# Optimization experiments

Measured on AMD Instinct MI355X. Metric: run time of the kernel, lower is better.

Reference implementation:

```python
import jax, jax.numpy as jnp
import numpy as np

N_NODES = 200000  # graph size
D = 128           # feature dim == out_size
N1 = 81920        # layer-1 node set size
B = 8192          # batch size
K = 10            # num_sample neighbors


def setup_inputs() -> dict:
    key = jax.random.key(0)
    k = jax.random.split(key, 7)
    raw_features = jax.random.normal(k[0], (N_NODES, D), dtype=jnp.float32)
    # xavier-like scale for weights [out, 2*in]
    W1 = jax.random.normal(k[1], (D, 2 * D), dtype=jnp.float32) * (1.0 / np.sqrt(2 * D))
    W2 = jax.random.normal(k[2], (D, 2 * D), dtype=jnp.float32) * (1.0 / np.sqrt(2 * D))
    layer1_nodes = jax.random.randint(k[3], (N1,), 0, N_NODES)
    neigh0_idx = jax.random.randint(k[4], (N1, K), 0, N_NODES)
    map_batch = jax.random.randint(k[5], (B,), 0, N1)
    neigh1_idx = jax.random.randint(k[6], (B, K), 0, N1)
    return {
        "raw_features": raw_features,
        "W1": W1,
        "W2": W2,
        "layer1_nodes": layer1_nodes,
        "neigh0_idx": neigh0_idx,
        "map_batch": map_batch,
        "neigh1_idx": neigh1_idx,
    }


def _sage_layer(self_feats, agg_feats, W):
    # combined = cat([self, agg], dim=1); relu(W @ combined.T).T == relu(combined @ W.T)
    combined = jnp.concatenate([self_feats, agg_feats], axis=1)
    return jax.nn.relu(combined @ W.T)


def reference(raw_features, W1, W2, layer1_nodes, neigh0_idx, map_batch, neigh1_idx):
    # Layer 1: aggregate raw features over K sampled neighbors (MEAN), gcn=False
    agg0 = jnp.mean(raw_features[neigh0_idx], axis=1)        # [N1, D]
    self0 = raw_features[layer1_nodes]                        # [N1, D]
    h1 = _sage_layer(self0, agg0, W1)                         # [N1, D]
    # Layer 2: aggregate layer-1 embeddings for the batch nodes
    agg1 = jnp.mean(h1[neigh1_idx], axis=1)                   # [B, D]
    self1 = h1[map_batch]                                     # [B, D]
    h2 = _sage_layer(self1, agg1, W2)                         # [B, D]
    return h2
```

## Files before the change

### kernel.cpp

```cpp
#include <hip/hip_runtime.h>
#include <stdint.h>

#define D 128
#define K_NEI 10
#define TILE_M 64

typedef __bf16 bf16x8 __attribute__((ext_vector_type(8)));
typedef float f32x4 __attribute__((ext_vector_type(4)));

__device__ __forceinline__ uint32_t f2bf(float f) {
    union { float f; uint32_t u; } v; v.f = f;
    uint32_t u = v.u;
    return (u + 0x7FFFu + ((u >> 16) & 1u)) >> 16;
}
__device__ __forceinline__ float bf2f(uint32_t h) {
    union { uint32_t u; float f; } v; v.u = h << 16; return v.f;
}
__device__ __forceinline__ uint32_t pack2(float a, float b) {
    return f2bf(a) | (f2bf(b) << 16);
}

template <bool FEATS_F32>
__global__ void build_A(const void* __restrict__ feats_,
                        const int* __restrict__ self_idx,
                        const int* __restrict__ neigh_idx,
                        uint16_t* __restrict__ A, int M)
{
    const int t = blockIdx.x * 256 + threadIdx.x;
    const int i = t >> 4;
    const int j = t & 15;
    if (i >= M) return;

    const float*    ff = (const float*)feats_;
    const uint16_t* fb = (const uint16_t*)feats_;

    {
        int node = self_idx[i];
        uint4 o;
        if (FEATS_F32) {
            const float* src = ff + (size_t)node * D + j * 8;
            f32x4 a = *(const f32x4*)src;
            f32x4 b = *(const f32x4*)(src + 4);
            o.x = pack2(a[0], a[1]); o.y = pack2(a[2], a[3]);
            o.z = pack2(b[0], b[1]); o.w = pack2(b[2], b[3]);
        } else {
            o = *(const uint4*)(fb + (size_t)node * D + j * 8);
        }
        *(uint4*)(A + (size_t)i * 256 + j * 8) = o;
    }

    const int* nrow = neigh_idx + (size_t)i * K_NEI;
    int idx[K_NEI];
    #pragma unroll
    for (int k = 0; k < K_NEI; ++k) idx[k] = nrow[k];

    float s0=0,s1=0,s2=0,s3=0,s4=0,s5=0,s6=0,s7=0;
    #pragma unroll
    for (int k = 0; k < K_NEI; ++k) {
        if (FEATS_F32) {
            const float* src = ff + (size_t)idx[k] * D + j * 8;
            f32x4 a = *(const f32x4*)src;
            f32x4 b = *(const f32x4*)(src + 4);
            s0 += a[0]; s1 += a[1]; s2 += a[2]; s3 += a[3];
            s4 += b[0]; s5 += b[1]; s6 += b[2]; s7 += b[3];
        } else {
            uint4 v = *(const uint4*)(fb + (size_t)idx[k] * D + j * 8);
            s0 += bf2f(v.x & 0xFFFFu); s1 += bf2f(v.x >> 16);
            s2 += bf2f(v.y & 0xFFFFu); s3 += bf2f(v.y >> 16);
            s4 += bf2f(v.z & 0xFFFFu); s5 += bf2f(v.z >> 16);
            s6 += bf2f(v.w & 0xFFFFu); s7 += bf2f(v.w >> 16);
        }
    }
    const float inv = 0.1f;
    uint4 o;
    o.x = pack2(s0 * inv, s1 * inv);
    o.y = pack2(s2 * inv, s3 * inv);
    o.z = pack2(s4 * inv, s5 * inv);
    o.w = pack2(s6 * inv, s7 * inv);
    *(uint4*)(A + (size_t)i * 256 + 128 + j * 8) = o;
}

template <bool OUT_F32>
__global__ void gemm_relu(const uint16_t* __restrict__ A,
                          const float* __restrict__ W,
                          void* __restrict__ out_)
{
    __shared__ __align__(16) uint16_t Alds[TILE_M * 128];
    __shared__ __align__(16) uint16_t Wlds[128 * 128];

    const int tid  = threadIdx.x;
    const int wave = tid >> 6;
    const int lane = tid & 63;
    const int r16  = lane & 15;
    const int q    = lane >> 4;
    const int G    = blockIdx.x * TILE_M;

    f32x4 acc[8];
    #pragma unroll
    for (int nt = 0; nt < 8; ++nt) acc[nt] = (f32x4){0.f, 0.f, 0.f, 0.f};

    for (int half = 0; half < 2; ++half) {
        #pragma unroll
        for (int it = 0; it < 8; ++it) {
            int t = it * 256 + tid;
            int j = t >> 4, c = t & 15;
            const float* src = W + (size_t)j * 256 + half * 128 + c * 8;
            f32x4 w0 = *(const f32x4*)(src);
            f32x4 w1 = *(const f32x4*)(src + 4);
            uint4 o;
            o.x = pack2(w0[0], w0[1]); o.y = pack2(w0[2], w0[3]);
            o.z = pack2(w1[0], w1[1]); o.w = pack2(w1[2], w1[3]);
            int cs = c ^ (j & 15);
            *(uint4*)(Wlds + j * 128 + cs * 8) = o;
        }
        #pragma unroll
        for (int it = 0; it < 4; ++it) {
            int t = it * 256 + tid;
            int n = t >> 4, c = t & 15;
            uint4 v = *(const uint4*)(A + (size_t)(G + n) * 256 + half * 128 + c * 8);
            int cs = c ^ (n & 15);
            *(uint4*)(Alds + n * 128 + cs * 8) = v;
        }
        __syncthreads();

        #pragma unroll
        for (int ks = 0; ks < 4; ++ks) {
            int cidx = ks * 4 + q;
            bf16x8 a = *(const bf16x8*)(Alds + (wave * 16 + r16) * 128 + ((cidx ^ r16) * 8));
            bf16x8 b[8];
            #pragma unroll
            for (int nt = 0; nt < 8; ++nt) {
                int jj = nt * 16 + r16;
                b[nt] = *(const bf16x8*)(Wlds + jj * 128 + ((cidx ^ r16) * 8));
            }
            #pragma unroll
            for (int nt = 0; nt < 8; ++nt)
                acc[nt] = __builtin_amdgcn_mfma_f32_16x16x32_bf16(a, b[nt], acc[nt], 0, 0, 0);
        }
        __syncthreads();
    }

    const int row_base = G + wave * 16 + q * 4;
    #pragma unroll
    for (int nt = 0; nt < 8; ++nt) {
        int col = nt * 16 + r16;
        #pragma unroll
        for (int r = 0; r < 4; ++r) {
            float v = acc[nt][r];
            v = v > 0.f ? v : 0.f;
            if (OUT_F32) ((float*)out_)[(size_t)(row_base + r) * D + col] = v;
            else ((uint16_t*)out_)[(size_t)(row_base + r) * D + col] = (uint16_t)f2bf(v);
        }
    }
}

template <bool FEATS_F32, bool OUT_F32>
__global__ void sage_layer(const void* __restrict__ feats_,
                           const float* __restrict__ W,
                           const int* __restrict__ self_idx,
                           const int* __restrict__ neigh_idx,
                           void* __restrict__ out_)
{
    __shared__ __align__(16) uint16_t Alds[TILE_M * 128];
    __shared__ __align__(16) uint16_t Wlds[128 * 128];

    const int tid  = threadIdx.x;
    const int wave = tid >> 6;
    const int lane = tid & 63;
    const int r16  = lane & 15;
    const int q    = lane >> 4;
    const int G    = blockIdx.x * TILE_M;

    const float*    feats_f = (const float*)feats_;
    const uint16_t* feats_b = (const uint16_t*)feats_;

    f32x4 acc[8];
    #pragma unroll
    for (int nt = 0; nt < 8; ++nt) acc[nt] = (f32x4){0.f, 0.f, 0.f, 0.f};

    for (int half = 0; half < 2; ++half) {
        #pragma unroll
        for (int it = 0; it < 8; ++it) {
            int t = it * 256 + tid;
            int j = t >> 4, c = t & 15;
            const float* src = W + (size_t)j * 256 + half * 128 + c * 8;
            f32x4 w0 = *(const f32x4*)(src);
            f32x4 w1 = *(const f32x4*)(src + 4);
            uint4 o;
            o.x = pack2(w0[0], w0[1]); o.y = pack2(w0[2], w0[3]);
            o.z = pack2(w1[0], w1[1]); o.w = pack2(w1[2], w1[3]);
            int cs = c ^ (j & 15);
            *(uint4*)(Wlds + j * 128 + cs * 8) = o;
        }
        if (half == 0) {
            #pragma unroll
            for (int it = 0; it < 4; ++it) {
                int t = it * 256 + tid;
                int n = t >> 4, c = t & 15;
                int node = self_idx[G + n];
                uint4 o;
                if (FEATS_F32) {
                    const float* src = feats_f + (size_t)node * D + c * 8;
                    f32x4 f0 = *(const f32x4*)(src);
                    f32x4 f1 = *(const f32x4*)(src + 4);
                    o.x = pack2(f0[0], f0[1]); o.y = pack2(f0[2], f0[3]);
                    o.z = pack2(f1[0], f1[1]); o.w = pack2(f1[2], f1[3]);
                } else {
                    o = *(const uint4*)(feats_b + (size_t)node * D + c * 8);
                }
                int cs = c ^ (n & 15);
                *(uint4*)(Alds + n * 128 + cs * 8) = o;
            }
        } else {
            #pragma unroll
            for (int it = 0; it < 4; ++it) {
                int t = it * 256 + tid;
                int n = t >> 4, c = t & 15;
                const int* nrow = neigh_idx + (size_t)(G + n) * K_NEI;
                float s0=0,s1=0,s2=0,s3=0,s4=0,s5=0,s6=0,s7=0;
                #pragma unroll
                for (int k = 0; k < K_NEI; ++k) {
                    if (FEATS_F32) {
                        const float* src = feats_f + (size_t)nrow[k] * D + c * 8;
                        f32x4 f0 = *(const f32x4*)(src);
                        f32x4 f1 = *(const f32x4*)(src + 4);
                        s0 += f0[0]; s1 += f0[1]; s2 += f0[2]; s3 += f0[3];
                        s4 += f1[0]; s5 += f1[1]; s6 += f1[2]; s7 += f1[3];
                    } else {
                        uint4 v = *(const uint4*)(feats_b + (size_t)nrow[k] * D + c * 8);
                        s0 += bf2f(v.x & 0xFFFFu); s1 += bf2f(v.x >> 16);
                        s2 += bf2f(v.y & 0xFFFFu); s3 += bf2f(v.y >> 16);
                        s4 += bf2f(v.z & 0xFFFFu); s5 += bf2f(v.z >> 16);
                        s6 += bf2f(v.w & 0xFFFFu); s7 += bf2f(v.w >> 16);
                    }
                }
                const float inv = 0.1f;
                uint4 o;
                o.x = pack2(s0 * inv, s1 * inv);
                o.y = pack2(s2 * inv, s3 * inv);
                o.z = pack2(s4 * inv, s5 * inv);
                o.w = pack2(s6 * inv, s7 * inv);
                int cs = c ^ (n & 15);
                *(uint4*)(Alds + n * 128 + cs * 8) = o;
            }
        }
        __syncthreads();

        #pragma unroll
        for (int ks = 0; ks < 4; ++ks) {
            int cidx = ks * 4 + q;
            bf16x8 a = *(const bf16x8*)(Alds + (wave * 16 + r16) * 128 + ((cidx ^ r16) * 8));
            bf16x8 b[8];
            #pragma unroll
            for (int nt = 0; nt < 8; ++nt) {
                int jj = nt * 16 + r16;
                b[nt] = *(const bf16x8*)(Wlds + jj * 128 + ((cidx ^ r16) * 8));
            }
            #pragma unroll
            for (int nt = 0; nt < 8; ++nt)
                acc[nt] = __builtin_amdgcn_mfma_f32_16x16x32_bf16(a, b[nt], acc[nt], 0, 0, 0);
        }
        __syncthreads();
    }

    const int row_base = G + wave * 16 + q * 4;
    #pragma unroll
    for (int nt = 0; nt < 8; ++nt) {
        int col = nt * 16 + r16;
        #pragma unroll
        for (int r = 0; r < 4; ++r) {
            float v = acc[nt][r];
            v = v > 0.f ? v : 0.f;
            if (OUT_F32) ((float*)out_)[(size_t)(row_base + r) * D + col] = v;
            else ((uint16_t*)out_)[(size_t)(row_base + r) * D + col] = (uint16_t)f2bf(v);
        }
    }
}

extern "C" void kernel_launch(void* const* d_in, const int* in_sizes, int n_in,
                              void* d_out, int out_size, void* d_ws, size_t ws_size,
                              hipStream_t stream) {
    const float* raw = (const float*)d_in[0];
    const float* W1  = (const float*)d_in[1];
    const float* W2  = (const float*)d_in[2];
    const int* layer1_nodes = (const int*)d_in[3];
    const int* neigh0       = (const int*)d_in[4];
    const int* map_batch    = (const int*)d_in[5];
    const int* neigh1       = (const int*)d_in[6];

    const int N1 = in_sizes[3];
    const int B  = in_sizes[5];

    const size_t needed = (size_t)N1 * 256 * 2 + (size_t)N1 * 128 * 2 + (size_t)B * 256 * 2;

    if (ws_size >= needed) {
        uint16_t* A1 = (uint16_t*)d_ws;
        uint16_t* h1 = A1 + (size_t)N1 * 256;
        uint16_t* A2 = h1 + (size_t)N1 * 128;

        build_A<true ><<<(N1 * 16 + 255) / 256, 256, 0, stream>>>(raw, layer1_nodes, neigh0, A1, N1);
        gemm_relu<false><<<N1 / TILE_M, 256, 0, stream>>>(A1, W1, h1);
        build_A<false><<<(B * 16 + 255) / 256, 256, 0, stream>>>(h1, map_batch, neigh1, A2, B);
        gemm_relu<true ><<<B / TILE_M, 256, 0, stream>>>(A2, W2, d_out);
    } else {
        uint16_t* h1 = (uint16_t*)d_ws;
        sage_layer<true,  false><<<N1 / TILE_M, 256, 0, stream>>>(raw, W1, layer1_nodes, neigh0, h1);
        sage_layer<false, true ><<<B  / TILE_M, 256, 0, stream>>>(h1,  W2, map_batch,    neigh1, d_out);
    }
}
```

Baseline: 246.6 us.

## Transform node features before aggregating, then gather and combine projected rows

Splits each SAGE layer into a dense GEMM that projects every source node's features with both halves of W (self and neighbour) into a bf16 table P. A light combine kernel then gathers the self half and averages the neighbour half over the K sampled nodes, applying ReLU. This shrinks each gathered row from 512 B of fp32 to 256 B of bf16 and removes the materialised concatenated A matrix. In exchange, layer 1 now does a GEMM over all 200k nodes instead of the 81920 layer-1 nodes, and layer 2 over all N1 rows instead of the 8192 batch rows. It also needs a larger workspace and adds a bf16 rounding of the projected values before averaging.

New measurement: 244.6 us. No clear change (-0.8%).

```diff
diff --git a/kernel.cpp b/kernel.cpp
--- a/kernel.cpp
+++ b/kernel.cpp
@@ -18,6 +18,147 @@
 }
 __device__ __forceinline__ uint32_t pack2(float a, float b) {
     return f2bf(a) | (f2bf(b) << 16);
+}
+
+__global__ void convert_W(const float* __restrict__ W, uint16_t* __restrict__ Wb)
+{
+    int t = blockIdx.x * 256 + threadIdx.x;
+    int c = t >> 4, j = t & 15;
+    const float* src = W + (size_t)(c & 127) * 256 + (c >> 7) * 128 + j * 8;
+    f32x4 a = *(const f32x4*)src;
+    f32x4 b = *(const f32x4*)(src + 4);
+    uint4 o;
+    o.x = pack2(a[0], a[1]); o.y = pack2(a[2], a[3]);
+    o.z = pack2(b[0], b[1]); o.w = pack2(b[2], b[3]);
+    *(uint4*)(Wb + (size_t)c * 128 + j * 8) = o;
+}
+
+template <bool A_F32>
+__global__ void gemm_P(const void* __restrict__ Asrc_,
+                       const uint16_t* __restrict__ Wb,
+                       uint16_t* __restrict__ P)
+{
+    __shared__ __align__(16) uint16_t Alds[TILE_M * 128];
+    __shared__ __align__(16) uint16_t Wlds[128 * 128];
+
+    const int tid  = threadIdx.x;
+    const int wave = tid >> 6;
+    const int lane = tid & 63;
+    const int r16  = lane & 15;
+    const int q    = lane >> 4;
+    const int G    = blockIdx.x * TILE_M;
+
+    #pragma unroll
+    for (int it = 0; it < 4; ++it) {
+        int t = it * 256 + tid;
+        int n = t >> 4, c = t & 15;
+        uint4 o;
+        if (A_F32) {
+            const float* src = (const float*)Asrc_ + (size_t)(G + n) * D + c * 8;
+            f32x4 a = *(const f32x4*)src;
+            f32x4 b = *(const f32x4*)(src + 4);
+            o.x = pack2(a[0], a[1]); o.y = pack2(a[2], a[3]);
+            o.z = pack2(b[0], b[1]); o.w = pack2(b[2], b[3]);
+        } else {
+            o = *(const uint4*)((const uint16_t*)Asrc_ + (size_t)(G + n) * D + c * 8);
+        }
+        int cs = c ^ (n & 15);
+        *(uint4*)(Alds + n * 128 + cs * 8) = o;
+    }
+
+    f32x4 acc[2][8];
+    #pragma unroll
+    for (int h = 0; h < 2; ++h)
+        #pragma unroll
+        for (int nt = 0; nt < 8; ++nt) acc[h][nt] = (f32x4){0.f, 0.f, 0.f, 0.f};
+
+    for (int h = 0; h < 2; ++h) {
+        #pragma unroll
+        for (int it = 0; it < 8; ++it) {
+            int t = it * 256 + tid;
+            int j = t >> 4, c = t & 15;
+            uint4 v = *(const uint4*)(Wb + (size_t)(h * 128 + j) * 128 + c * 8);
+            int cs = c ^ (j & 15);
+            *(uint4*)(Wlds + j * 128 + cs * 8) = v;
+        }
+        __syncthreads();
+
+        #pragma unroll
+        for (int ks = 0; ks < 4; ++ks) {
+            int cidx = ks * 4 + q;
+            bf16x8 a = *(const bf16x8*)(Alds + (wave * 16 + r16) * 128 + ((cidx ^ r16) * 8));
+            bf16x8 b[8];
+            #pragma unroll
+            for (int nt = 0; nt < 8; ++nt) {
+                int jj = nt * 16 + r16;
+                b[nt] = *(const bf16x8*)(Wlds + jj * 128 + ((cidx ^ r16) * 8));
+            }
+            #pragma unroll
+            for (int nt = 0; nt < 8; ++nt)
+                acc[h][nt] = __builtin_amdgcn_mfma_f32_16x16x32_bf16(a, b[nt], acc[h][nt], 0, 0, 0);
+        }
+        __syncthreads();
+    }
+
+    const int row_base = G + wave * 16 + q * 4;
+    #pragma unroll
+    for (int h = 0; h < 2; ++h)
+        #pragma unroll
+        for (int nt = 0; nt < 8; ++nt) {
+            int col = h * 128 + nt * 16 + r16;
+            #pragma unroll
+            for (int r = 0; r < 4; ++r)
+                P[(size_t)(row_base + r) * 256 + col] = (uint16_t)f2bf(acc[h][nt][r]);
+        }
+}
+
+template <bool OUT_F32>
+__global__ void combine(const uint16_t* __restrict__ P,
+                        const int* __restrict__ self_idx,
+                        const int* __restrict__ neigh_idx,
+                        void* __restrict__ out_, int M)
+{
+    const int t = blockIdx.x * 256 + threadIdx.x;
+    const int i = t >> 4;
+    const int j = t & 15;
+    if (i >= M) return;
+
+    uint4 sv = *(const uint4*)(P + (size_t)self_idx[i] * 256 + j * 8);
+
+    const int* nrow = neigh_idx + (size_t)i * K_NEI;
+    int idx[K_NEI];
+    #pragma unroll
+    for (int k = 0; k < K_NEI; ++k) idx[k] = nrow[k];
+
+    float s0=0,s1=0,s2=0,s3=0,s4=0,s5=0,s6=0,s7=0;
+    #pragma unroll
+    for (int k = 0; k < K_NEI; ++k) {
+        uint4 v = *(const uint4*)(P + (size_t)idx[k] * 256 + 128 + j * 8);
+        s0 += bf2f(v.x & 0xFFFFu); s1 += bf2f(v.x >> 16);
+        s2 += bf2f(v.y & 0xFFFFu); s3 += bf2f(v.y >> 16);
+        s4 += bf2f(v.z & 0xFFFFu); s5 += bf2f(v.z >> 16);
+        s6 += bf2f(v.w & 0xFFFFu); s7 += bf2f(v.w >> 16);
+    }
+    const float inv = 0.1f;
+    float r0 = bf2f(sv.x & 0xFFFFu) + s0 * inv, r1 = bf2f(sv.x >> 16) + s1 * inv;
+    float r2 = bf2f(sv.y & 0xFFFFu) + s2 * inv, r3 = bf2f(sv.y >> 16) + s3 * inv;
+    float r4 = bf2f(sv.z & 0xFFFFu) + s4 * inv, r5 = bf2f(sv.z >> 16) + s5 * inv;
+    float r6 = bf2f(sv.w & 0xFFFFu) + s6 * inv, r7 = bf2f(sv.w >> 16) + s7 * inv;
+    r0 = r0 > 0.f ? r0 : 0.f; r1 = r1 > 0.f ? r1 : 0.f;
+    r2 = r2 > 0.f ? r2 : 0.f; r3 = r3 > 0.f ? r3 : 0.f;
+    r4 = r4 > 0.f ? r4 : 0.f; r5 = r5 > 0.f ? r5 : 0.f;
+    r6 = r6 > 0.f ? r6 : 0.f; r7 = r7 > 0.f ? r7 : 0.f;
+
+    if (OUT_F32) {
+        float* dst = (float*)out_ + (size_t)i * D + j * 8;
+        *(f32x4*)dst       = (f32x4){r0, r1, r2, r3};
+        *(f32x4*)(dst + 4) = (f32x4){r4, r5, r6, r7};
+    } else {
+        uint4 o;
+        o.x = pack2(r0, r1); o.y = pack2(r2, r3);
+        o.z = pack2(r4, r5); o.w = pack2(r6, r7);
+        *(uint4*)((uint16_t*)out_ + (size_t)i * D + j * 8) = o;
+    }
 }
 
 template <bool FEATS_F32>
@@ -154,129 +295,6 @@
     }
 }
 
-template <bool FEATS_F32, bool OUT_F32>
-__global__ void sage_layer(const void* __restrict__ feats_,
-                           const float* __restrict__ W,
-                           const int* __restrict__ self_idx,
-                           const int* __restrict__ neigh_idx,
-                           void* __restrict__ out_)
-{
-    __shared__ __align__(16) uint16_t Alds[TILE_M * 128];
-    __shared__ __align__(16) uint16_t Wlds[128 * 128];
-
-    const int tid  = threadIdx.x;
-    const int wave = tid >> 6;
-    const int lane = tid & 63;
-    const int r16  = lane & 15;
-    const int q    = lane >> 4;
-    const int G    = blockIdx.x * TILE_M;
-
-    const float*    feats_f = (const float*)feats_;
-    const uint16_t* feats_b = (const uint16_t*)feats_;
-
-    f32x4 acc[8];
-    #pragma unroll
-    for (int nt = 0; nt < 8; ++nt) acc[nt] = (f32x4){0.f, 0.f, 0.f, 0.f};
-
-    for (int half = 0; half < 2; ++half) {
-        #pragma unroll
-        for (int it = 0; it < 8; ++it) {
-            int t = it * 256 + tid;
-            int j = t >> 4, c = t & 15;
-            const float* src = W + (size_t)j * 256 + half * 128 + c * 8;
-            f32x4 w0 = *(const f32x4*)(src);
-            f32x4 w1 = *(const f32x4*)(src + 4);
-            uint4 o;
-            o.x = pack2(w0[0], w0[1]); o.y = pack2(w0[2], w0[3]);
-            o.z = pack2(w1[0], w1[1]); o.w = pack2(w1[2], w1[3]);
-            int cs = c ^ (j & 15);
-            *(uint4*)(Wlds + j * 128 + cs * 8) = o;
-        }
-        if (half == 0) {
-            #pragma unroll
-            for (int it = 0; it < 4; ++it) {
-                int t = it * 256 + tid;
-                int n = t >> 4, c = t & 15;
-                int node = self_idx[G + n];
-                uint4 o;
-                if (FEATS_F32) {
-                    const float* src = feats_f + (size_t)node * D + c * 8;
-                    f32x4 f0 = *(const f32x4*)(src);
-                    f32x4 f1 = *(const f32x4*)(src + 4);
-                    o.x = pack2(f0[0], f0[1]); o.y = pack2(f0[2], f0[3]);
-                    o.z = pack2(f1[0], f1[1]); o.w = pack2(f1[2], f1[3]);
-                } else {
-                    o = *(const uint4*)(feats_b + (size_t)node * D + c * 8);
-                }
-                int cs = c ^ (n & 15);
-                *(uint4*)(Alds + n * 128 + cs * 8) = o;
-            }
-        } else {
-            #pragma unroll
-            for (int it = 0; it < 4; ++it) {
-                int t = it * 256 + tid;
-                int n = t >> 4, c = t & 15;
-                const int* nrow = neigh_idx + (size_t)(G + n) * K_NEI;
-                float s0=0,s1=0,s2=0,s3=0,s4=0,s5=0,s6=0,s7=0;
-                #pragma unroll
-                for (int k = 0; k < K_NEI; ++k) {
-                    if (FEATS_F32) {
-                        const float* src = feats_f + (size_t)nrow[k] * D + c * 8;
-                        f32x4 f0 = *(const f32x4*)(src);
-                        f32x4 f1 = *(const f32x4*)(src + 4);
-                        s0 += f0[0]; s1 += f0[1]; s2 += f0[2]; s3 += f0[3];
-                        s4 += f1[0]; s5 += f1[1]; s6 += f1[2]; s7 += f1[3];
-                    } else {
-                        uint4 v = *(const uint4*)(feats_b + (size_t)nrow[k] * D + c * 8);
-                        s0 += bf2f(v.x & 0xFFFFu); s1 += bf2f(v.x >> 16);
-                        s2 += bf2f(v.y & 0xFFFFu); s3 += bf2f(v.y >> 16);
-                        s4 += bf2f(v.z & 0xFFFFu); s5 += bf2f(v.z >> 16);
-                        s6 += bf2f(v.w & 0xFFFFu); s7 += bf2f(v.w >> 16);
-                    }
-                }
-                const float inv = 0.1f;
-                uint4 o;
-                o.x = pack2(s0 * inv, s1 * inv);
-                o.y = pack2(s2 * inv, s3 * inv);
-                o.z = pack2(s4 * inv, s5 * inv);
-                o.w = pack2(s6 * inv, s7 * inv);
-                int cs = c ^ (n & 15);
-                *(uint4*)(Alds + n * 128 + cs * 8) = o;
-            }
-        }
-        __syncthreads();
-
-        #pragma unroll
-        for (int ks = 0; ks < 4; ++ks) {
-            int cidx = ks * 4 + q;
-            bf16x8 a = *(const bf16x8*)(Alds + (wave * 16 + r16) * 128 + ((cidx ^ r16) * 8));
-            bf16x8 b[8];
-            #pragma unroll
-            for (int nt = 0; nt < 8; ++nt) {
-                int jj = nt * 16 + r16;
-                b[nt] = *(const bf16x8*)(Wlds + jj * 128 + ((cidx ^ r16) * 8));
-            }
-            #pragma unroll
-            for (int nt = 0; nt < 8; ++nt)
-                acc[nt] = __builtin_amdgcn_mfma_f32_16x16x32_bf16(a, b[nt], acc[nt], 0, 0, 0);
-        }
-        __syncthreads();
-    }
-
-    const int row_base = G + wave * 16 + q * 4;
-    #pragma unroll
-    for (int nt = 0; nt < 8; ++nt) {
-        int col = nt * 16 + r16;
-        #pragma unroll
-        for (int r = 0; r < 4; ++r) {
-            float v = acc[nt][r];
-            v = v > 0.f ? v : 0.f;
-            if (OUT_F32) ((float*)out_)[(size_t)(row_base + r) * D + col] = v;
-            else ((uint16_t*)out_)[(size_t)(row_base + r) * D + col] = (uint16_t)f2bf(v);
-        }
-    }
-}
-
 extern "C" void kernel_launch(void* const* d_in, const int* in_sizes, int n_in,
                               void* d_out, int out_size, void* d_ws, size_t ws_size,
                               hipStream_t stream) {
@@ -288,12 +306,33 @@
     const int* map_batch    = (const int*)d_in[5];
     const int* neigh1       = (const int*)d_in[6];
 
+    const int N_NODES = in_sizes[0] / D;
     const int N1 = in_sizes[3];
     const int B  = in_sizes[5];
 
-    const size_t needed = (size_t)N1 * 256 * 2 + (size_t)N1 * 128 * 2 + (size_t)B * 256 * 2;
-
-    if (ws_size >= needed) {
+    const size_t szP  = (size_t)N_NODES * 256 * 2;
+    const size_t szQ  = (size_t)N1 * 256 * 2;
+    const size_t szH1 = (size_t)N1 * 128 * 2;
+    const size_t szW  = 256 * 128 * 2;
+    const size_t needA = (szP > szQ ? szP : szQ) + szH1 + 2 * szW;
+
+    if (ws_size >= needA && (N_NODES % TILE_M) == 0 && (N1 % TILE_M) == 0) {
+        uint16_t* Pbuf = (uint16_t*)d_ws;
+        uint16_t* h1   = (uint16_t*)((char*)d_ws + (szP > szQ ? szP : szQ));
+        uint16_t* W1b  = h1 + (size_t)N1 * 128;
+        uint16_t* W2b  = W1b + 256 * 128;
+
+        convert_W<<<16, 256, 0, stream>>>(W1, W1b);
+        convert_W<<<16, 256, 0, stream>>>(W2, W2b);
+        gemm_P<true ><<<N_NODES / TILE_M, 256, 0, stream>>>(raw, W1b, Pbuf);
+        combine<false><<<(N1 * 16 + 255) / 256, 256, 0, stream>>>(Pbuf, layer1_nodes, neigh0, h1, N1);
+        gemm_P<false><<<N1 / TILE_M, 256, 0, stream>>>(h1, W2b, Pbuf);
+        combine<true ><<<(B * 16 + 255) / 256, 256, 0, stream>>>(Pbuf, map_batch, neigh1, d_out, B);
+        return;
+    }
+
+    const size_t needB = (size_t)N1 * 256 * 2 + (size_t)N1 * 128 * 2 + (size_t)B * 256 * 2;
+    if (ws_size >= needB) {
         uint16_t* A1 = (uint16_t*)d_ws;
         uint16_t* h1 = A1 + (size_t)N1 * 256;
         uint16_t* A2 = h1 + (size_t)N1 * 128;
@@ -302,9 +341,5 @@
         gemm_relu<false><<<N1 / TILE_M, 256, 0, stream>>>(A1, W1, h1);
         build_A<false><<<(B * 16 + 255) / 256, 256, 0, stream>>>(h1, map_batch, neigh1, A2, B);
         gemm_relu<true ><<<B / TILE_M, 256, 0, stream>>>(A2, W2, d_out);
-    } else {
-        uint16_t* h1 = (uint16_t*)d_ws;
-        sage_layer<true,  false><<<N1 / TILE_M, 256, 0, stream>>>(raw, W1, layer1_nodes, neigh0, h1);
-        sage_layer<false, true ><<<B  / TILE_M, 256, 0, stream>>>(h1,  W2, map_batch,    neigh1, d_out);
-    }
-}
+    }
+}
```
